# Kernel optimization log

Hardware: AMD Instinct MI355X
Metric: run time of the kernel (lower is better)

## Reference

```python
import jax, jax.numpy as jnp
import numpy as np

B, T, C, H, D, G, V, M = 4, 1024, 768, 12, 4, 4, 32000, 1024
S = C // H


def layernorm(x, g, b, eps=1e-5):
    mu = jnp.mean(x, -1, keepdims=True)
    var = jnp.mean(jnp.square(x - mu), -1, keepdims=True)
    return (x - mu) * jax.lax.rsqrt(var + eps) * g + b


def setup_inputs() -> dict:
    key = jax.random.key(0)
    ks = jax.random.split(key, 12)
    std = 0.02  # matches _init_weights normal(0, 0.02)
    n = lambda k, sh: jax.random.normal(k, sh, jnp.float32) * std
    return {
        'x': jax.random.randint(ks[0], (B, T), 0, V),
        'y': jax.random.randint(ks[1], (B, T), 0, V),
        'wordemb': n(ks[2], (V, C)),
        'posemb': n(ks[3], (M, C)),
        'Wq': n(ks[4], (D, C, C)),
        'Wk': n(ks[5], (D, C, C)),
        'Wv': n(ks[6], (D, C, C)),
        'Wo': n(ks[7], (D, C, C)),
        'bo': jnp.zeros((D, C), jnp.float32),
        'ln1_g': jnp.ones((D, C), jnp.float32),
        'ln1_b': jnp.zeros((D, C), jnp.float32),
        'W1': n(ks[8], (D, C, G * C)),
        'b1': jnp.zeros((D, G * C), jnp.float32),
        'W2': n(ks[9], (D, G * C, C)),
        'b2': jnp.zeros((D, C), jnp.float32),
        'ln2_g': jnp.ones((D, C), jnp.float32),
        'ln2_b': jnp.zeros((D, C), jnp.float32),
        'Wl': n(ks[10], (C, V)),
        'bl': jnp.zeros((V,), jnp.float32),
    }


def _forward(x, y, wordemb, posemb, Wq, Wk, Wv, Wo, bo, ln1_g, ln1_b,
             W1, b1, W2, b2, ln2_g, ln2_b, Wl, bl):
    b, t = x.shape
    emb = wordemb[x] + posemb[:t][None, :, :]  # (b,t,c)
    causal = jnp.tril(jnp.ones((t, t), bool))

    def block(h_in, p):
        wq, wk, wv, wo, bo_, g1, be1, w1, b1_, w2, b2_, g2, be2 = p
        q = (h_in @ wq).reshape(b, t, H, S)
        k = (h_in @ wk).reshape(b, t, H, S)
        v = (h_in @ wv).reshape(b, t, H, S)
        # note: original scales by sqrt(channels), NOT sqrt(head_dim)
        w = jnp.einsum('bqhs,bkhs->bhqk', q, k) / jnp.sqrt(jnp.float32(C))
        w = jnp.where(causal, w, -jnp.inf)
        w = jax.nn.softmax(w, axis=-1)
        att = jnp.einsum('bhqk,bkhs->bqhs', w, v).reshape(b, t, C)
        att = att @ wo + bo_
        h1 = h_in + layernorm(att, g1, be1)   # x + norm1(attn(x))
        ff = jax.nn.relu(h1 @ w1 + b1_) @ w2 + b2_
        h2 = h1 + layernorm(ff, g2, be2)      # x + norm2(ff(x)); dropout=0
        return h2, None

    hfin, _ = jax.lax.scan(
        block, emb,
        (Wq, Wk, Wv, Wo, bo, ln1_g, ln1_b, W1, b1, W2, b2, ln2_g, ln2_b))
    logits = hfin @ Wl + bl  # (b,t,v)
    logp = jax.nn.log_softmax(logits, axis=-1)
    nll = -jnp.take_along_axis(logp, y[..., None], axis=-1)[..., 0]
    loss = jnp.mean(nll)
    return logits, loss


def reference(x, y, wordemb, posemb, Wq, Wk, Wv, Wo, bo, ln1_g, ln1_b,
              W1, b1, W2, b2, ln2_g, ln2_b, Wl, bl):
    return _forward(x, y, wordemb, posemb, Wq, Wk, Wv, Wo, bo, ln1_g, ln1_b,
                    W1, b1, W2, b2, ln2_g, ln2_b, Wl, bl)
```

## Files before the change

kernel.cpp:

```cpp
#include <hip/hip_runtime.h>

#define Bn 4
#define Tn 1024
#define Cn 768
#define Hn 12
#define Dn 4
#define Vn 32000
#define BTn (Bn*Tn)
#define NBX 250

typedef __attribute__((ext_vector_type(8))) short short8;
typedef __attribute__((ext_vector_type(4))) float f32x4;

__device__ __forceinline__ unsigned short f2bf(float f) {
  union { float f; unsigned u; } v; v.f = f;
  unsigned r = v.u + 0x7fffu + ((v.u >> 16) & 1u);
  return (unsigned short)(r >> 16);
}

__device__ __forceinline__ void gload_lds16(const void* g, void* l) {
  __builtin_amdgcn_global_load_lds(
      (const __attribute__((address_space(1))) void*)g,
      (__attribute__((address_space(3))) void*)l, 16, 0, 0);
}

__global__ __launch_bounds__(256)
void transpose_bf16_kernel(const float* __restrict__ src0, unsigned short* __restrict__ dst0,
                           int K, int N, size_t sStride, size_t dStride) {
  const float* src = src0 + blockIdx.z * sStride;
  unsigned short* dst = dst0 + blockIdx.z * dStride;
  __shared__ float tile[32][33];
  const int tx = threadIdx.x, ty = threadIdx.y;
  const int n0 = blockIdx.x * 32, k0 = blockIdx.y * 32;
#pragma unroll
  for (int i = 0; i < 4; ++i)
    tile[ty + i*8][tx] = src[(size_t)(k0 + ty + i*8) * N + n0 + tx];
  __syncthreads();
#pragma unroll
  for (int i = 0; i < 4; ++i)
    dst[(size_t)(n0 + ty + i*8) * K + k0 + tx] = f2bf(tile[tx][ty + i*8]);
}

__global__ __launch_bounds__(256)
void embed_kernel(const int* __restrict__ x, const float* __restrict__ wordemb,
                  const float* __restrict__ posemb, float* __restrict__ h,
                  unsigned short* __restrict__ hb) {
  int i4 = blockIdx.x * 256 + threadIdx.x;
  int row = i4 / (Cn/4), c4 = i4 % (Cn/4);
  int t = row & (Tn - 1);
  int tok = x[row];
  float4 a = ((const float4*)wordemb)[(size_t)tok * (Cn/4) + c4];
  float4 p = ((const float4*)posemb)[(size_t)t * (Cn/4) + c4];
  float4 s; s.x = a.x+p.x; s.y = a.y+p.y; s.z = a.z+p.z; s.w = a.w+p.w;
  ((float4*)h)[i4] = s;
  ushort4 u; u.x = f2bf(s.x); u.y = f2bf(s.y); u.z = f2bf(s.z); u.w = f2bf(s.w);
  ((ushort4*)hb)[i4] = u;
}

__global__ __launch_bounds__(256, 2)
void gemm_l(const unsigned short* __restrict__ A, const unsigned short* __restrict__ Bt,
            const float* __restrict__ bias, float* __restrict__ Cf,
            unsigned short* __restrict__ Cb, int M, int N, int K, int relu,
            unsigned short* __restrict__ vTp) {
  __shared__ __align__(16) unsigned short lds[2*16384];
  const int tid = threadIdx.x;
  const int gx = gridDim.x;
  const int flat = blockIdx.x + gx*blockIdx.y;
  const int chq = (gx * gridDim.y) >> 3;
  const int swz = (flat & 7)*chq + (flat >> 3);
  const int by = swz % gx, bx = swz / gx;
  const int lane = tid & 63, w = tid >> 6;
  const int wr = w >> 1, wc = w & 1;
  const int lr = lane & 15, lq = lane >> 4;
  const int xm = (lr >> 1) & 3;
  const int sslot = (lane & 3) ^ ((lane >> 3) & 3);
  const int NT = K >> 6;

  f32x4 acc[4][4];
#pragma unroll
  for (int i = 0; i < 4; ++i)
#pragma unroll
    for (int j = 0; j < 4; ++j)
      acc[i][j] = (f32x4){0.f, 0.f, 0.f, 0.f};

  const unsigned short* aS = A  + (size_t)(by*128 + w*16 + (lane>>2))*K + sslot*8;
  const unsigned short* bS = Bt + (size_t)(bx*128 + w*16 + (lane>>2))*K + sslot*8;

  auto stA = [&](int t) {
    unsigned short* d = &lds[(t&1)*16384];
    const int k0 = t*64;
#pragma unroll
    for (int kh = 0; kh < 2; ++kh)
#pragma unroll
      for (int i = 0; i < 2; ++i)
        gload_lds16(aS + k0 + kh*32 + (size_t)i*64*K, d + kh*4096 + (i*64 + w*16)*32);
  };
  auto stB = [&](int t) {
    unsigned short* d = &lds[(t&1)*16384 + 8192];
    const int k0 = t*64;
#pragma unroll
    for (int kh = 0; kh < 2; ++kh)
#pragma unroll
      for (int i = 0; i < 2; ++i)
        gload_lds16(bS + k0 + kh*32 + (size_t)i*64*K, d + kh*4096 + (i*64 + w*16)*32);
  };
  auto rdA = [&](int t, int kh, short8* af) {
    const unsigned short* p = &lds[(t&1)*16384 + kh*4096];
#pragma unroll
    for (int mi = 0; mi < 4; ++mi)
      af[mi] = *(const short8*)&p[(wr*64 + mi*16 + lr)*32 + (lq ^ xm)*8];
  };
  auto rdB = [&](int t, int kh, short8* bf) {
    const unsigned short* p = &lds[(t&1)*16384 + 8192 + kh*4096];
#pragma unroll
    for (int nj = 0; nj < 4; ++nj)
      bf[nj] = *(const short8*)&p[(wc*64 + nj*16 + lr)*32 + (lq ^ xm)*8];
  };

  short8 af0[4], af1[4], bf0[4], bf1[4];
  stA(0); stB(0); stA(1);

  for (int t = 0; t < NT; ++t) {
    if (t + 1 < NT) { asm volatile("s_waitcnt vmcnt(4)" ::: "memory"); }
    else            { asm volatile("s_waitcnt vmcnt(0)" ::: "memory"); }
    __builtin_amdgcn_s_barrier();
    __builtin_amdgcn_sched_barrier(0);
    rdA(t, 0, af0); rdA(t, 1, af1); rdB(t, 0, bf0);
    if (t + 1 < NT) stB(t + 1);
    __builtin_amdgcn_s_barrier();
    __builtin_amdgcn_sched_barrier(0);
    __builtin_amdgcn_s_setprio(1);
#pragma unroll
    for (int i = 0; i < 4; ++i)
#pragma unroll
      for (int j = 0; j < 4; ++j)
        acc[i][j] = __builtin_amdgcn_mfma_f32_16x16x32_bf16(af0[i], bf0[j], acc[i][j], 0, 0, 0);
    __builtin_amdgcn_s_setprio(0);
    __builtin_amdgcn_s_barrier();
    rdB(t, 1, bf1);
    if (t + 2 < NT) stA(t + 2);
    __builtin_amdgcn_s_barrier();
    __builtin_amdgcn_sched_barrier(0);
    __builtin_amdgcn_s_setprio(1);
#pragma unroll
    for (int i = 0; i < 4; ++i)
#pragma unroll
      for (int j = 0; j < 4; ++j)
        acc[i][j] = __builtin_amdgcn_mfma_f32_16x16x32_bf16(af1[i], bf1[j], acc[i][j], 0, 0, 0);
    __builtin_amdgcn_s_setprio(0);
  }

  const bool isV = (vTp != nullptr) && (bx*128 >= 1536);
  if (!isV) {
#pragma unroll
    for (int mi = 0; mi < 4; ++mi)
#pragma unroll
      for (int nj = 0; nj < 4; ++nj)
#pragma unroll
        for (int r = 0; r < 4; ++r) {
          int grow = by*128 + wr*64 + mi*16 + lq*4 + r;
          int gcol = bx*128 + wc*64 + nj*16 + lr;
          float v = acc[mi][nj][r];
          if (bias) v += bias[gcol];
          if (relu) v = fmaxf(v, 0.f);
          size_t idx = (size_t)grow * N + gcol;
          if (Cf) Cf[idx] = v;
          if (Cb) Cb[idx] = f2bf(v);
        }
  } else {
    __syncthreads();
    unsigned short (*tile)[136] = (unsigned short (*)[136])lds;
#pragma unroll
    for (int mi = 0; mi < 4; ++mi)
#pragma unroll
      for (int nj = 0; nj < 4; ++nj)
#pragma unroll
        for (int r = 0; r < 4; ++r) {
          int lt = wr*64 + mi*16 + lq*4 + r;
          int ld = wc*64 + nj*16 + lr;
          tile[ld][lt] = f2bf(acc[mi][nj][r]);
        }
    __syncthreads();
    const int bq = (by*128) >> 10;
    const int t0 = (by*128) & 1023;
#pragma unroll
    for (int i = 0; i < 32; ++i) {
      int ld = w*32 + i;
      int gd = bx*128 + ld - 1536;
      int hh2 = gd >> 6, dd = gd & 63;
      ushort2 val = *(ushort2*)&tile[ld][2*lane];
      *(ushort2*)&vTp[((size_t)((bq*Hn + hh2)*64 + dd))*Tn + t0 + 2*lane] = val;
    }
  }
}

__global__ __launch_bounds__(256, 2)
void gemm_vocab(const unsigned short* __restrict__ A, const unsigned short* __restrict__ Bt,
                const float* __restrict__ bias, float* __restrict__ Cf,
                float2* __restrict__ lsepart) {
  constexpr int K = 768, N = Vn, NT = 12;
  __shared__ __align__(16) unsigned short lds[2*16384];
  const int tid = threadIdx.x;
  const int gx = gridDim.x;
  const int flat = blockIdx.x + gx*blockIdx.y;
  const int chq = (gx * gridDim.y) >> 3;
  const int swz = (flat & 7)*chq + (flat >> 3);
  const int by = swz % gx, bx = swz / gx;
  const int lane = tid & 63, w = tid >> 6;
  const int wr = w >> 1, wc = w & 1;
  const int lr = lane & 15, lq = lane >> 4;
  const int xm = (lr >> 1) & 3;
  const int sslot = (lane & 3) ^ ((lane >> 3) & 3);

  f32x4 acc[4][4];
#pragma unroll
  for (int i = 0; i < 4; ++i)
#pragma unroll
    for (int j = 0; j < 4; ++j)
      acc[i][j] = (f32x4){0.f, 0.f, 0.f, 0.f};

  const unsigned short* aS = A  + (size_t)(by*128 + w*16 + (lane>>2))*K + sslot*8;
  const unsigned short* bS = Bt + (size_t)(bx*128 + w*16 + (lane>>2))*K + sslot*8;

  auto stA = [&](int t) {
    unsigned short* d = &lds[(t&1)*16384];
    const int k0 = t*64;
#pragma unroll
    for (int kh = 0; kh < 2; ++kh)
#pragma unroll
      for (int i = 0; i < 2; ++i)
        gload_lds16(aS + k0 + kh*32 + (size_t)i*64*K, d + kh*4096 + (i*64 + w*16)*32);
  };
  auto stB = [&](int t) {
    unsigned short* d = &lds[(t&1)*16384 + 8192];
    const int k0 = t*64;
#pragma unroll
    for (int kh = 0; kh < 2; ++kh)
#pragma unroll
      for (int i = 0; i < 2; ++i)
        gload_lds16(bS + k0 + kh*32 + (size_t)i*64*K, d + kh*4096 + (i*64 + w*16)*32);
  };
  auto rdA = [&](int t, int kh, short8* af) {
    const unsigned short* p = &lds[(t&1)*16384 + kh*4096];
#pragma unroll
    for (int mi = 0; mi < 4; ++mi)
      af[mi] = *(const short8*)&p[(wr*64 + mi*16 + lr)*32 + (lq ^ xm)*8];
  };
  auto rdB = [&](int t, int kh, short8* bf) {
    const unsigned short* p = &lds[(t&1)*16384 + 8192 + kh*4096];
#pragma unroll
    for (int nj = 0; nj < 4; ++nj)
      bf[nj] = *(const short8*)&p[(wc*64 + nj*16 + lr)*32 + (lq ^ xm)*8];
  };

  short8 af0[4], af1[4], bf0[4], bf1[4];
  stA(0); stB(0); stA(1);

  for (int t = 0; t < NT; ++t) {
    if (t + 1 < NT) { asm volatile("s_waitcnt vmcnt(4)" ::: "memory"); }
    else            { asm volatile("s_waitcnt vmcnt(0)" ::: "memory"); }
    __builtin_amdgcn_s_barrier();
    __builtin_amdgcn_sched_barrier(0);
    rdA(t, 0, af0); rdA(t, 1, af1); rdB(t, 0, bf0);
    if (t + 1 < NT) stB(t + 1);
    __builtin_amdgcn_s_barrier();
    __builtin_amdgcn_sched_barrier(0);
    __builtin_amdgcn_s_setprio(1);
#pragma unroll
    for (int i = 0; i < 4; ++i)
#pragma unroll
      for (int j = 0; j < 4; ++j)
        acc[i][j] = __builtin_amdgcn_mfma_f32_16x16x32_bf16(af0[i], bf0[j], acc[i][j], 0, 0, 0);
    __builtin_amdgcn_s_setprio(0);
    __builtin_amdgcn_s_barrier();
    rdB(t, 1, bf1);
    if (t + 2 < NT) stA(t + 2);
    __builtin_amdgcn_s_barrier();
    __builtin_amdgcn_sched_barrier(0);
    __builtin_amdgcn_s_setprio(1);
#pragma unroll
    for (int i = 0; i < 4; ++i)
#pragma unroll
      for (int j = 0; j < 4; ++j)
        acc[i][j] = __builtin_amdgcn_mfma_f32_16x16x32_bf16(af1[i], bf1[j], acc[i][j], 0, 0, 0);
    __builtin_amdgcn_s_setprio(0);
  }

  __syncthreads();
  float2* part = (float2*)lds;
#pragma unroll
  for (int mi = 0; mi < 4; ++mi)
#pragma unroll
    for (int r = 0; r < 4; ++r) {
      float v[4]; float m = -3.0e38f;
#pragma unroll
      for (int nj = 0; nj < 4; ++nj) {
        int gcol = bx*128 + wc*64 + nj*16 + lr;
        float val = acc[mi][nj][r] + bias[gcol];
        v[nj] = val;
        m = fmaxf(m, val);
      }
      int prow = wr*64 + mi*16 + lq*4 + r;
      int grow = by*128 + prow;
      float* crow = Cf + (size_t)grow * N + bx*128 + wc*64 + lr;
#pragma unroll
      for (int nj = 0; nj < 4; ++nj) crow[nj*16] = v[nj];
      float s = 0.f;
#pragma unroll
      for (int nj = 0; nj < 4; ++nj) s += __expf(v[nj] - m);
#pragma unroll
      for (int mask = 1; mask < 16; mask <<= 1) {
        float m2 = __shfl_xor(m, mask), s2 = __shfl_xor(s, mask);
        float mn = fmaxf(m, m2);
        s = s*__expf(m - mn) + s2*__expf(m2 - mn);
        m = mn;
      }
      if (lr == 0) part[prow*2 + wc] = make_float2(m, s);
    }
  __syncthreads();
  if (tid < 128) {
    float2 p0 = part[tid*2], p1 = part[tid*2 + 1];
    float mn = fmaxf(p0.x, p1.x);
    float s = p0.y*__expf(p0.x - mn) + p1.y*__expf(p1.x - mn);
    lsepart[(size_t)(by*128 + tid)*NBX + bx] = make_float2(mn, s);
  }
}

__global__ __launch_bounds__(512)
void attn_mfma_kernel(const unsigned short* __restrict__ qkvb,
                      const unsigned short* __restrict__ vT,
                      unsigned short* __restrict__ attb) {
  const int qb = blockIdx.x, hh = blockIdx.y, b = blockIdx.z;
  const int t = threadIdx.x;
  const int lane = t & 63, w = t >> 6;
  const int lr = lane & 15, lg = lane >> 4;
  const float scale = 0.03608439182435161f;

  __shared__ unsigned short Ks[2][64*64];
  __shared__ unsigned short Vs[2][64*64];
  __shared__ unsigned short Ps[8][16][72];

  const int R0 = qb*128 + w*16;
  const int myDiag = R0 >> 6;
  const int NTILES = 2*qb + 2;

  const unsigned short* qsrc = qkvb + (size_t)(b*Tn + R0 + lr)*2304 + hh*64 + lg*8;
  short8 qa0 = *(const short8*)(qsrc);
  short8 qa1 = *(const short8*)(qsrc + 32);

  f32x4 acc[4];
#pragma unroll
  for (int dt = 0; dt < 4; ++dt) acc[dt] = (f32x4){0.f,0.f,0.f,0.f};
  float m_run[4], l_run[4];
#pragma unroll
  for (int r = 0; r < 4; ++r) { m_run[r] = -1e30f; l_run[r] = 0.f; }

  const int sr = (t & 255) >> 2, c2 = t & 3;

  auto stage = [&](int kvb) {
    const int buf = kvb & 1;
    int s0 = (2*c2) ^ (sr & 7), s1 = (2*c2 + 1) ^ (sr & 7);
    if (t < 256) {
      const unsigned short* ksrc = qkvb + (size_t)(b*Tn + kvb*64 + sr)*2304 + 768 + hh*64 + c2*16;
      short8 k0 = *(const short8*)ksrc;
      short8 k1 = *(const short8*)(ksrc + 8);
      *(short8*)&Ks[buf][sr*64 + s0*8] = k0;
      *(short8*)&Ks[buf][sr*64 + s1*8] = k1;
    } else {
      const unsigned short* vsrc = vT + ((size_t)((b*Hn + hh)*64 + sr))*Tn + kvb*64 + c2*16;
      short8 vv0 = *(const short8*)vsrc;
      short8 vv1 = *(const short8*)(vsrc + 8);
      *(short8*)&Vs[buf][sr*64 + s0*8] = vv0;
      *(short8*)&Vs[buf][sr*64 + s1*8] = vv1;
    }
  };

  stage(0);
  __syncthreads();

  for (int kvb = 0; kvb < NTILES; ++kvb) {
    if (kvb + 1 < NTILES) stage(kvb + 1);
    const int buf = kvb & 1;

    if (kvb <= myDiag) {
      f32x4 s[4];
#pragma unroll
      for (int kt = 0; kt < 4; ++kt) {
        int krow = kt*16 + lr;
        short8 kf0 = *(const short8*)&Ks[buf][krow*64 + ((0 + lg) ^ (krow & 7))*8];
        short8 kf1 = *(const short8*)&Ks[buf][krow*64 + ((4 + lg) ^ (krow & 7))*8];
        f32x4 a = (f32x4){0.f,0.f,0.f,0.f};
        a = __builtin_amdgcn_mfma_f32_16x16x32_bf16(qa0, kf0, a, 0, 0, 0);
        a = __builtin_amdgcn_mfma_f32_16x16x32_bf16(qa1, kf1, a, 0, 0, 0);
        s[kt] = a;
      }
      const bool diag = (kvb == myDiag);
#pragma unroll
      for (int kt = 0; kt < 4; ++kt)
#pragma unroll
        for (int r = 0; r < 4; ++r) {
          float v = s[kt][r] * scale;
          if (diag && (kt*16 + lr > (w & 3)*16 + lg*4 + r)) v = -1e30f;
          s[kt][r] = v;
        }
#pragma unroll
      for (int r = 0; r < 4; ++r) {
        float m = fmaxf(fmaxf(s[0][r], s[1][r]), fmaxf(s[2][r], s[3][r]));
        m = fmaxf(m, __shfl_xor(m, 1));
        m = fmaxf(m, __shfl_xor(m, 2));
        m = fmaxf(m, __shfl_xor(m, 4));
        m = fmaxf(m, __shfl_xor(m, 8));
        float mn = fmaxf(m_run[r], m);
        float corr = __expf(m_run[r] - mn);
        m_run[r] = mn;
        float ps = 0.f;
#pragma unroll
        for (int kt = 0; kt < 4; ++kt) {
          float p = __expf(s[kt][r] - mn);
          s[kt][r] = p;
          ps += p;
        }
        ps += __shfl_xor(ps, 1);
        ps += __shfl_xor(ps, 2);
        ps += __shfl_xor(ps, 4);
        ps += __shfl_xor(ps, 8);
        l_run[r] = l_run[r] * corr + ps;
#pragma unroll
        for (int dt = 0; dt < 4; ++dt) acc[dt][r] *= corr;
      }
#pragma unroll
      for (int kt = 0; kt < 4; ++kt)
#pragma unroll
        for (int r = 0; r < 4; ++r)
          Ps[w][lg*4 + r][kt*16 + lr] = f2bf(s[kt][r]);
      short8 pa0 = *(const short8*)&Ps[w][lr][lg*8];
      short8 pa1 = *(const short8*)&Ps[w][lr][32 + lg*8];
#pragma unroll
      for (int dt = 0; dt < 4; ++dt) {
        int drow = dt*16 + lr;
        short8 vf0 = *(const short8*)&Vs[buf][drow*64 + ((0 + lg) ^ (drow & 7))*8];
        short8 vf1 = *(const short8*)&Vs[buf][drow*64 + ((4 + lg) ^ (drow & 7))*8];
        acc[dt] = __builtin_amdgcn_mfma_f32_16x16x32_bf16(pa0, vf0, acc[dt], 0, 0, 0);
        acc[dt] = __builtin_amdgcn_mfma_f32_16x16x32_bf16(pa1, vf1, acc[dt], 0, 0, 0);
      }
    }
    __syncthreads();
  }

  unsigned short* obase = attb + (size_t)(b*Tn + R0)*768 + hh*64;
#pragma unroll
  for (int dt = 0; dt < 4; ++dt)
#pragma unroll
    for (int r = 0; r < 4; ++r) {
      float v = acc[dt][r] / l_run[r];
      obase[(size_t)(lg*4 + r)*768 + dt*16 + lr] = f2bf(v);
    }
}

__global__ __launch_bounds__(256)
void ln_res_kernel(const float* __restrict__ x, float* __restrict__ h,
                   unsigned short* __restrict__ hb, const float* __restrict__ g,
                   const float* __restrict__ bb) {
  const int lane = threadIdx.x & 63;
  const int row = blockIdx.x*4 + (threadIdx.x >> 6);
  const float4* xr4 = (const float4*)(x + (size_t)row * Cn);
  float4 v[3];
  float s1 = 0.f, s2 = 0.f;
#pragma unroll
  for (int j = 0; j < 3; ++j) {
    v[j] = xr4[lane + j*64];
    s1 += v[j].x + v[j].y + v[j].z + v[j].w;
    s2 += v[j].x*v[j].x + v[j].y*v[j].y + v[j].z*v[j].z + v[j].w*v[j].w;
  }
#pragma unroll
  for (int m = 1; m < 64; m <<= 1) { s1 += __shfl_xor(s1, m); s2 += __shfl_xor(s2, m); }
  float mu = s1 * (1.f/768.f);
  float var = s2 * (1.f/768.f) - mu*mu;
  float rs = rsqrtf(var + 1e-5f);
  float4* hr4 = (float4*)(h + (size_t)row * Cn);
  ushort4* hb4 = (ushort4*)(hb + (size_t)row * Cn);
  const float4* g4 = (const float4*)g;
  const float4* b4 = (const float4*)bb;
#pragma unroll
  for (int j = 0; j < 3; ++j) {
    int c = lane + j*64;
    float4 hv = hr4[c], gv = g4[c], bv = b4[c];
    float4 y;
    y.x = hv.x + (v[j].x - mu)*rs*gv.x + bv.x;
    y.y = hv.y + (v[j].y - mu)*rs*gv.y + bv.y;
    y.z = hv.z + (v[j].z - mu)*rs*gv.z + bv.z;
    y.w = hv.w + (v[j].w - mu)*rs*gv.w + bv.w;
    hr4[c] = y;
    ushort4 u; u.x = f2bf(y.x); u.y = f2bf(y.y); u.z = f2bf(y.z); u.w = f2bf(y.w);
    hb4[c] = u;
  }
}

__global__ __launch_bounds__(256)
void loss_part_kernel(const float2* __restrict__ part, const float* __restrict__ logits,
                      const int* __restrict__ y, float* __restrict__ loss_rows) {
  const int row = blockIdx.x, tid = threadIdx.x;
  float m = -3.0e38f, s = 0.f;
  if (tid < NBX) { float2 p = part[(size_t)row*NBX + tid]; m = p.x; s = p.y; }
#pragma unroll
  for (int mask = 1; mask < 64; mask <<= 1) {
    float m2 = __shfl_xor(m, mask), s2 = __shfl_xor(s, mask);
    float mn = fmaxf(m, m2);
    s = s*__expf(m - mn) + s2*__expf(m2 - mn);
    m = mn;
  }
  __shared__ float mw[4], sw[4];
  if ((tid & 63) == 0) { mw[tid >> 6] = m; sw[tid >> 6] = s; }
  __syncthreads();
  if (tid == 0) {
#pragma unroll
    for (int i = 1; i < 4; ++i) {
      float mn = fmaxf(m, mw[i]);
      s = s*__expf(m - mn) + sw[i]*__expf(mw[i] - mn);
      m = mn;
    }
    loss_rows[row] = m + __logf(s) - logits[(size_t)row*Vn + y[row]];
  }
}

__global__ __launch_bounds__(256)
void loss_reduce_kernel(const float* __restrict__ loss_rows, float* __restrict__ out) {
  const int tid = threadIdx.x;
  float s = 0.f;
  for (int j = 0; j < BTn/256; ++j) s += loss_rows[tid + j*256];
  __shared__ float red[256];
  red[tid] = s; __syncthreads();
  for (int st = 128; st > 0; st >>= 1) {
    if (tid < st) red[tid] += red[tid+st];
    __syncthreads();
  }
  if (tid == 0) out[0] = red[0] * (1.f/(float)BTn);
}

extern "C" void kernel_launch(void* const* d_in, const int* in_sizes, int n_in,
                              void* d_out, int out_size, void* d_ws, size_t ws_size,
                              hipStream_t stream) {
  const int*   x       = (const int*)  d_in[0];
  const int*   y       = (const int*)  d_in[1];
  const float* wordemb = (const float*)d_in[2];
  const float* posemb  = (const float*)d_in[3];
  const float* Wq      = (const float*)d_in[4];
  const float* Wk      = (const float*)d_in[5];
  const float* Wv      = (const float*)d_in[6];
  const float* Wo      = (const float*)d_in[7];
  const float* bo      = (const float*)d_in[8];
  const float* ln1_g   = (const float*)d_in[9];
  const float* ln1_b   = (const float*)d_in[10];
  const float* W1      = (const float*)d_in[11];
  const float* b1      = (const float*)d_in[12];
  const float* W2      = (const float*)d_in[13];
  const float* b2      = (const float*)d_in[14];
  const float* ln2_g   = (const float*)d_in[15];
  const float* ln2_b   = (const float*)d_in[16];
  const float* Wl      = (const float*)d_in[17];
  const float* bl      = (const float*)d_in[18];

  char* ws = (char*)d_ws;
  size_t off = 0;
  auto alloc = [&](size_t bytes) -> char* {
    char* p = ws + off;
    off += (bytes + 255) & ~(size_t)255;
    return p;
  };
  unsigned short* wqkvT = (unsigned short*)alloc((size_t)Dn*2304*768*2);
  unsigned short* woT   = (unsigned short*)alloc((size_t)Dn*768*768*2);
  unsigned short* w1T   = (unsigned short*)alloc((size_t)Dn*3072*768*2);
  unsigned short* w2T   = (unsigned short*)alloc((size_t)Dn*768*3072*2);
  unsigned short* wlT   = (unsigned short*)alloc((size_t)Vn*768*2);
  float*          h     = (float*)alloc((size_t)BTn*Cn*4);
  unsigned short* hb    = (unsigned short*)alloc((size_t)BTn*Cn*2);
  unsigned short* qkvb  = (unsigned short*)alloc((size_t)BTn*3072*2);
  unsigned short* vTb   = (unsigned short*)alloc((size_t)Bn*Hn*64*Tn*2);
  unsigned short* attb  = (unsigned short*)alloc((size_t)BTn*Cn*2);
  float*          tmp   = (float*)alloc((size_t)BTn*Cn*4);
  float*          loss_rows = (float*)alloc((size_t)BTn*4);
  float2*         lsepart   = (float2*)alloc((size_t)BTn*NBX*8);
  unsigned short* ff1b  = qkvb;

  dim3 tb(32, 8);
  transpose_bf16_kernel<<<dim3(24,24,Dn), tb, 0, stream>>>(Wq, wqkvT,             Cn, Cn, (size_t)Cn*Cn, (size_t)2304*768);
  transpose_bf16_kernel<<<dim3(24,24,Dn), tb, 0, stream>>>(Wk, wqkvT + 768*768,   Cn, Cn, (size_t)Cn*Cn, (size_t)2304*768);
  transpose_bf16_kernel<<<dim3(24,24,Dn), tb, 0, stream>>>(Wv, wqkvT + 1536*768,  Cn, Cn, (size_t)Cn*Cn, (size_t)2304*768);
  transpose_bf16_kernel<<<dim3(24,24,Dn), tb, 0, stream>>>(Wo, woT,               Cn, Cn, (size_t)Cn*Cn, (size_t)768*768);
  transpose_bf16_kernel<<<dim3(96,24,Dn), tb, 0, stream>>>(W1, w1T, 768, 3072, (size_t)768*3072, (size_t)3072*768);
  transpose_bf16_kernel<<<dim3(24,96,Dn), tb, 0, stream>>>(W2, w2T, 3072, 768, (size_t)3072*768, (size_t)768*3072);
  transpose_bf16_kernel<<<dim3(1000,24,1), tb, 0, stream>>>(Wl, wlT, 768, Vn, 0, 0);

  embed_kernel<<<(BTn*Cn/4)/256, 256, 0, stream>>>(x, wordemb, posemb, h, hb);

  for (int d = 0; d < Dn; ++d) {
    gemm_l<<<dim3(BTn/128, 2304/128), 256, 0, stream>>>(
        hb, wqkvT + (size_t)d*2304*768, nullptr, nullptr, qkvb, BTn, 2304, 768, 0, vTb);
    attn_mfma_kernel<<<dim3(Tn/128, Hn, Bn), 512, 0, stream>>>(qkvb, vTb, attb);
    gemm_l<<<dim3(BTn/128, 768/128), 256, 0, stream>>>(
        attb, woT + (size_t)d*768*768, bo + (size_t)d*768, tmp, nullptr, BTn, 768, 768, 0, nullptr);
    ln_res_kernel<<<BTn/4, 256, 0, stream>>>(tmp, h, hb, ln1_g + (size_t)d*768, ln1_b + (size_t)d*768);
    gemm_l<<<dim3(BTn/128, 3072/128), 256, 0, stream>>>(
        hb, w1T + (size_t)d*3072*768, b1 + (size_t)d*3072, nullptr, ff1b, BTn, 3072, 768, 1, nullptr);
    gemm_l<<<dim3(BTn/128, 768/128), 256, 0, stream>>>(
        ff1b, w2T + (size_t)d*768*3072, b2 + (size_t)d*768, tmp, nullptr, BTn, 768, 3072, 0, nullptr);
    ln_res_kernel<<<BTn/4, 256, 0, stream>>>(tmp, h, hb, ln2_g + (size_t)d*768, ln2_b + (size_t)d*768);
  }

  float* logits = (float*)d_out;
  gemm_vocab<<<dim3(32, 250), 256, 0, stream>>>(hb, wlT, bl, logits, lsepart);
  loss_part_kernel<<<BTn, 256, 0, stream>>>(lsepart, logits, y, loss_rows);
  loss_reduce_kernel<<<1, 256, 0, stream>>>(loss_rows, logits + (size_t)BTn*Vn);
}
```

Baseline: 1.483 ms.

## Shrink attention tiles, emit bf16 pre-LN outputs, remap vocab GEMM blocks per XCD

Attention now uses 64-row query blocks with 4 waves, so each block handles one KV diagonal and every thread stages both K and V. This removes the idle half-block work on the diagonal of the old 128-row blocks and gives more blocks. The Wo and W2 GEMMs now write bf16 instead of fp32, and the layernorm-residual kernel reads bf16, halving that intermediate traffic at some cost in precision. The vocab GEMM uses a 1D grid mapped so each XCD gets four contiguous row tiles, aiming for better L2 reuse of A.

```diff
diff --git a/kernel.cpp b/kernel.cpp
--- a/kernel.cpp
+++ b/kernel.cpp
@@ -16,6 +16,9 @@
   union { float f; unsigned u; } v; v.f = f;
   unsigned r = v.u + 0x7fffu + ((v.u >> 16) & 1u);
   return (unsigned short)(r >> 16);
+}
+__device__ __forceinline__ float bf2f(unsigned short us) {
+  union { unsigned u; float f; } t; t.u = ((unsigned)us) << 16; return t.f;
 }
 
 __device__ __forceinline__ void gload_lds16(const void* g, void* l) {
@@ -201,11 +204,11 @@
   constexpr int K = 768, N = Vn, NT = 12;
   __shared__ __align__(16) unsigned short lds[2*16384];
   const int tid = threadIdx.x;
-  const int gx = gridDim.x;
-  const int flat = blockIdx.x + gx*blockIdx.y;
-  const int chq = (gx * gridDim.y) >> 3;
-  const int swz = (flat & 7)*chq + (flat >> 3);
-  const int by = swz % gx, bx = swz / gx;
+  const int bid = blockIdx.x;
+  const int xcd = bid & 7;
+  const int ii = bid >> 3;
+  const int by = xcd*4 + ii/250;
+  const int bx = ii % 250;
   const int lane = tid & 63, w = tid >> 6;
   const int wr = w >> 1, wc = w & 1;
   const int lr = lane & 15, lq = lane >> 4;
@@ -326,7 +329,7 @@
   }
 }
 
-__global__ __launch_bounds__(512)
+__global__ __launch_bounds__(256)
 void attn_mfma_kernel(const unsigned short* __restrict__ qkvb,
                       const unsigned short* __restrict__ vT,
                       unsigned short* __restrict__ attb) {
@@ -338,13 +341,9 @@
 
   __shared__ unsigned short Ks[2][64*64];
   __shared__ unsigned short Vs[2][64*64];
-  __shared__ unsigned short Ps[8][16][72];
-
-  const int R0 = qb*128 + w*16;
-  const int myDiag = R0 >> 6;
-  const int NTILES = 2*qb + 2;
-
-  const unsigned short* qsrc = qkvb + (size_t)(b*Tn + R0 + lr)*2304 + hh*64 + lg*8;
+  __shared__ unsigned short Ps[4][16][72];
+
+  const unsigned short* qsrc = qkvb + (size_t)(b*Tn + qb*64 + w*16 + lr)*2304 + hh*64 + lg*8;
   short8 qa0 = *(const short8*)(qsrc);
   short8 qa1 = *(const short8*)(qsrc + 32);
 
@@ -355,99 +354,94 @@
 #pragma unroll
   for (int r = 0; r < 4; ++r) { m_run[r] = -1e30f; l_run[r] = 0.f; }
 
-  const int sr = (t & 255) >> 2, c2 = t & 3;
+  const int sr = t >> 2, c2 = t & 3;
 
   auto stage = [&](int kvb) {
     const int buf = kvb & 1;
+    const unsigned short* ksrc = qkvb + (size_t)(b*Tn + kvb*64 + sr)*2304 + 768 + hh*64 + c2*16;
+    short8 k0 = *(const short8*)ksrc;
+    short8 k1 = *(const short8*)(ksrc + 8);
+    const unsigned short* vsrc = vT + ((size_t)((b*Hn + hh)*64 + sr))*Tn + kvb*64 + c2*16;
+    short8 vv0 = *(const short8*)vsrc;
+    short8 vv1 = *(const short8*)(vsrc + 8);
     int s0 = (2*c2) ^ (sr & 7), s1 = (2*c2 + 1) ^ (sr & 7);
-    if (t < 256) {
-      const unsigned short* ksrc = qkvb + (size_t)(b*Tn + kvb*64 + sr)*2304 + 768 + hh*64 + c2*16;
-      short8 k0 = *(const short8*)ksrc;
-      short8 k1 = *(const short8*)(ksrc + 8);
-      *(short8*)&Ks[buf][sr*64 + s0*8] = k0;
-      *(short8*)&Ks[buf][sr*64 + s1*8] = k1;
-    } else {
-      const unsigned short* vsrc = vT + ((size_t)((b*Hn + hh)*64 + sr))*Tn + kvb*64 + c2*16;
-      short8 vv0 = *(const short8*)vsrc;
-      short8 vv1 = *(const short8*)(vsrc + 8);
-      *(short8*)&Vs[buf][sr*64 + s0*8] = vv0;
-      *(short8*)&Vs[buf][sr*64 + s1*8] = vv1;
-    }
+    *(short8*)&Ks[buf][sr*64 + s0*8] = k0;
+    *(short8*)&Ks[buf][sr*64 + s1*8] = k1;
+    *(short8*)&Vs[buf][sr*64 + s0*8] = vv0;
+    *(short8*)&Vs[buf][sr*64 + s1*8] = vv1;
   };
 
   stage(0);
   __syncthreads();
 
-  for (int kvb = 0; kvb < NTILES; ++kvb) {
-    if (kvb + 1 < NTILES) stage(kvb + 1);
+  for (int kvb = 0; kvb <= qb; ++kvb) {
+    if (kvb < qb) stage(kvb + 1);
     const int buf = kvb & 1;
 
-    if (kvb <= myDiag) {
-      f32x4 s[4];
+    f32x4 s[4];
+#pragma unroll
+    for (int kt = 0; kt < 4; ++kt) {
+      int krow = kt*16 + lr;
+      short8 kf0 = *(const short8*)&Ks[buf][krow*64 + ((0 + lg) ^ (krow & 7))*8];
+      short8 kf1 = *(const short8*)&Ks[buf][krow*64 + ((4 + lg) ^ (krow & 7))*8];
+      f32x4 a = (f32x4){0.f,0.f,0.f,0.f};
+      a = __builtin_amdgcn_mfma_f32_16x16x32_bf16(qa0, kf0, a, 0, 0, 0);
+      a = __builtin_amdgcn_mfma_f32_16x16x32_bf16(qa1, kf1, a, 0, 0, 0);
+      s[kt] = a;
+    }
+    const bool diag = (kvb == qb);
+#pragma unroll
+    for (int kt = 0; kt < 4; ++kt)
+#pragma unroll
+      for (int r = 0; r < 4; ++r) {
+        float v = s[kt][r] * scale;
+        if (diag && (kt*16 + lr > w*16 + lg*4 + r)) v = -1e30f;
+        s[kt][r] = v;
+      }
+#pragma unroll
+    for (int r = 0; r < 4; ++r) {
+      float m = fmaxf(fmaxf(s[0][r], s[1][r]), fmaxf(s[2][r], s[3][r]));
+      m = fmaxf(m, __shfl_xor(m, 1));
+      m = fmaxf(m, __shfl_xor(m, 2));
+      m = fmaxf(m, __shfl_xor(m, 4));
+      m = fmaxf(m, __shfl_xor(m, 8));
+      float mn = fmaxf(m_run[r], m);
+      float corr = __expf(m_run[r] - mn);
+      m_run[r] = mn;
+      float ps = 0.f;
 #pragma unroll
       for (int kt = 0; kt < 4; ++kt) {
-        int krow = kt*16 + lr;
-        short8 kf0 = *(const short8*)&Ks[buf][krow*64 + ((0 + lg) ^ (krow & 7))*8];
-        short8 kf1 = *(const short8*)&Ks[buf][krow*64 + ((4 + lg) ^ (krow & 7))*8];
-        f32x4 a = (f32x4){0.f,0.f,0.f,0.f};
-        a = __builtin_amdgcn_mfma_f32_16x16x32_bf16(qa0, kf0, a, 0, 0, 0);
-        a = __builtin_amdgcn_mfma_f32_16x16x32_bf16(qa1, kf1, a, 0, 0, 0);
-        s[kt] = a;
+        float p = __expf(s[kt][r] - mn);
+        s[kt][r] = p;
+        ps += p;
       }
-      const bool diag = (kvb == myDiag);
-#pragma unroll
-      for (int kt = 0; kt < 4; ++kt)
-#pragma unroll
-        for (int r = 0; r < 4; ++r) {
-          float v = s[kt][r] * scale;
-          if (diag && (kt*16 + lr > (w & 3)*16 + lg*4 + r)) v = -1e30f;
-          s[kt][r] = v;
-        }
-#pragma unroll
-      for (int r = 0; r < 4; ++r) {
-        float m = fmaxf(fmaxf(s[0][r], s[1][r]), fmaxf(s[2][r], s[3][r]));
-        m = fmaxf(m, __shfl_xor(m, 1));
-        m = fmaxf(m, __shfl_xor(m, 2));
-        m = fmaxf(m, __shfl_xor(m, 4));
-        m = fmaxf(m, __shfl_xor(m, 8));
-        float mn = fmaxf(m_run[r], m);
-        float corr = __expf(m_run[r] - mn);
-        m_run[r] = mn;
-        float ps = 0.f;
-#pragma unroll
-        for (int kt = 0; kt < 4; ++kt) {
-          float p = __expf(s[kt][r] - mn);
-          s[kt][r] = p;
-          ps += p;
-        }
-        ps += __shfl_xor(ps, 1);
-        ps += __shfl_xor(ps, 2);
-        ps += __shfl_xor(ps, 4);
-        ps += __shfl_xor(ps, 8);
-        l_run[r] = l_run[r] * corr + ps;
-#pragma unroll
-        for (int dt = 0; dt < 4; ++dt) acc[dt][r] *= corr;
-      }
-#pragma unroll
-      for (int kt = 0; kt < 4; ++kt)
-#pragma unroll
-        for (int r = 0; r < 4; ++r)
-          Ps[w][lg*4 + r][kt*16 + lr] = f2bf(s[kt][r]);
-      short8 pa0 = *(const short8*)&Ps[w][lr][lg*8];
-      short8 pa1 = *(const short8*)&Ps[w][lr][32 + lg*8];
-#pragma unroll
-      for (int dt = 0; dt < 4; ++dt) {
-        int drow = dt*16 + lr;
-        short8 vf0 = *(const short8*)&Vs[buf][drow*64 + ((0 + lg) ^ (drow & 7))*8];
-        short8 vf1 = *(const short8*)&Vs[buf][drow*64 + ((4 + lg) ^ (drow & 7))*8];
-        acc[dt] = __builtin_amdgcn_mfma_f32_16x16x32_bf16(pa0, vf0, acc[dt], 0, 0, 0);
-        acc[dt] = __builtin_amdgcn_mfma_f32_16x16x32_bf16(pa1, vf1, acc[dt], 0, 0, 0);
-      }
+      ps += __shfl_xor(ps, 1);
+      ps += __shfl_xor(ps, 2);
+      ps += __shfl_xor(ps, 4);
+      ps += __shfl_xor(ps, 8);
+      l_run[r] = l_run[r] * corr + ps;
+#pragma unroll
+      for (int dt = 0; dt < 4; ++dt) acc[dt][r] *= corr;
+    }
+#pragma unroll
+    for (int kt = 0; kt < 4; ++kt)
+#pragma unroll
+      for (int r = 0; r < 4; ++r)
+        Ps[w][lg*4 + r][kt*16 + lr] = f2bf(s[kt][r]);
+    short8 pa0 = *(const short8*)&Ps[w][lr][lg*8];
+    short8 pa1 = *(const short8*)&Ps[w][lr][32 + lg*8];
+#pragma unroll
+    for (int dt = 0; dt < 4; ++dt) {
+      int drow = dt*16 + lr;
+      short8 vf0 = *(const short8*)&Vs[buf][drow*64 + ((0 + lg) ^ (drow & 7))*8];
+      short8 vf1 = *(const short8*)&Vs[buf][drow*64 + ((4 + lg) ^ (drow & 7))*8];
+      acc[dt] = __builtin_amdgcn_mfma_f32_16x16x32_bf16(pa0, vf0, acc[dt], 0, 0, 0);
+      acc[dt] = __builtin_amdgcn_mfma_f32_16x16x32_bf16(pa1, vf1, acc[dt], 0, 0, 0);
     }
     __syncthreads();
   }
 
-  unsigned short* obase = attb + (size_t)(b*Tn + R0)*768 + hh*64;
+  unsigned short* obase = attb + (size_t)(b*Tn + qb*64 + w*16)*768 + hh*64;
 #pragma unroll
   for (int dt = 0; dt < 4; ++dt)
 #pragma unroll
@@ -458,17 +452,18 @@
 }
 
 __global__ __launch_bounds__(256)
-void ln_res_kernel(const float* __restrict__ x, float* __restrict__ h,
+void ln_res_kernel(const unsigned short* __restrict__ xb, float* __restrict__ h,
                    unsigned short* __restrict__ hb, const float* __restrict__ g,
                    const float* __restrict__ bb) {
   const int lane = threadIdx.x & 63;
   const int row = blockIdx.x*4 + (threadIdx.x >> 6);
-  const float4* xr4 = (const float4*)(x + (size_t)row * Cn);
+  const ushort4* xr4 = (const ushort4*)(xb + (size_t)row * Cn);
   float4 v[3];
   float s1 = 0.f, s2 = 0.f;
 #pragma unroll
   for (int j = 0; j < 3; ++j) {
-    v[j] = xr4[lane + j*64];
+    ushort4 u = xr4[lane + j*64];
+    v[j].x = bf2f(u.x); v[j].y = bf2f(u.y); v[j].z = bf2f(u.z); v[j].w = bf2f(u.w);
     s1 += v[j].x + v[j].y + v[j].z + v[j].w;
     s2 += v[j].x*v[j].x + v[j].y*v[j].y + v[j].z*v[j].z + v[j].w*v[j].w;
   }
@@ -577,7 +572,7 @@
   unsigned short* qkvb  = (unsigned short*)alloc((size_t)BTn*3072*2);
   unsigned short* vTb   = (unsigned short*)alloc((size_t)Bn*Hn*64*Tn*2);
   unsigned short* attb  = (unsigned short*)alloc((size_t)BTn*Cn*2);
-  float*          tmp   = (float*)alloc((size_t)BTn*Cn*4);
+  unsigned short* tmpb  = (unsigned short*)alloc((size_t)BTn*Cn*2);
   float*          loss_rows = (float*)alloc((size_t)BTn*4);
   float2*         lsepart   = (float2*)alloc((size_t)BTn*NBX*8);
   unsigned short* ff1b  = qkvb;
@@ -596,19 +591,19 @@
   for (int d = 0; d < Dn; ++d) {
     gemm_l<<<dim3(BTn/128, 2304/128), 256, 0, stream>>>(
         hb, wqkvT + (size_t)d*2304*768, nullptr, nullptr, qkvb, BTn, 2304, 768, 0, vTb);
-    attn_mfma_kernel<<<dim3(Tn/128, Hn, Bn), 512, 0, stream>>>(qkvb, vTb, attb);
+    attn_mfma_kernel<<<dim3(Tn/64, Hn, Bn), 256, 0, stream>>>(qkvb, vTb, attb);
     gemm_l<<<dim3(BTn/128, 768/128), 256, 0, stream>>>(
-        attb, woT + (size_t)d*768*768, bo + (size_t)d*768, tmp, nullptr, BTn, 768, 768, 0, nullptr);
-    ln_res_kernel<<<BTn/4, 256, 0, stream>>>(tmp, h, hb, ln1_g + (size_t)d*768, ln1_b + (size_t)d*768);
+        attb, woT + (size_t)d*768*768, bo + (size_t)d*768, nullptr, tmpb, BTn, 768, 768, 0, nullptr);
+    ln_res_kernel<<<BTn/4, 256, 0, stream>>>(tmpb, h, hb, ln1_g + (size_t)d*768, ln1_b + (size_t)d*768);
     gemm_l<<<dim3(BTn/128, 3072/128), 256, 0, stream>>>(
         hb, w1T + (size_t)d*3072*768, b1 + (size_t)d*3072, nullptr, ff1b, BTn, 3072, 768, 1, nullptr);
     gemm_l<<<dim3(BTn/128, 768/128), 256, 0, stream>>>(
-        ff1b, w2T + (size_t)d*768*3072, b2 + (size_t)d*768, tmp, nullptr, BTn, 768, 3072, 0, nullptr);
-    ln_res_kernel<<<BTn/4, 256, 0, stream>>>(tmp, h, hb, ln2_g + (size_t)d*768, ln2_b + (size_t)d*768);
+        ff1b, w2T + (size_t)d*768*3072, b2 + (size_t)d*768, nullptr, tmpb, BTn, 768, 3072, 0, nullptr);
+    ln_res_kernel<<<BTn/4, 256, 0, stream>>>(tmpb, h, hb, ln2_g + (size_t)d*768, ln2_b + (size_t)d*768);
   }
 
   float* logits = (float*)d_out;
-  gemm_vocab<<<dim3(32, 250), 256, 0, stream>>>(hb, wlT, bl, logits, lsepart);
+  gemm_vocab<<<8000, 256, 0, stream>>>(hb, wlT, bl, logits, lsepart);
   loss_part_kernel<<<BTn, 256, 0, stream>>>(lsepart, logits, y, loss_rows);
   loss_reduce_kernel<<<1, 256, 0, stream>>>(loss_rows, logits + (size_t)BTn*Vn);
 }
```

New measurement: 1.310 ms. 11.6% less time.
